# Performance work log

Hardware: AMD Instinct MI355X
Metric: run time of the kernel (lower is better)

## Reference

```python
import jax, jax.numpy as jnp
import numpy as np

BATCH, IN, HID, NCLS = 4096, 2048, 8192, 1000

def setup_inputs() -> dict:
    key = jax.random.key(0)
    kx, kk, kg = jax.random.split(key, 3)
    x = jax.random.normal(kx, (BATCH, IN), dtype=jnp.float32)
    # torch nn.Linear weights: kohonen [HID, IN], grossberg [NCLS, HID], init U(-1, 1)
    Wk = jax.random.uniform(kk, (HID, IN), dtype=jnp.float32, minval=-1.0, maxval=1.0)
    Wg = jax.random.uniform(kg, (NCLS, HID), dtype=jnp.float32, minval=-1.0, maxval=1.0)
    return {"x": x, "Wk": Wk, "Wg": Wg}

def reference(x, Wk, Wg):
    # L2-normalize each row
    xn = x / jnp.linalg.norm(x, axis=1, keepdims=True)  # [B, IN]
    kohonen_out = jnp.einsum('bi,hi->bh', xn, Wk)        # [B, HID]
    idx = jnp.argmax(kohonen_out, axis=1)                # [B] winner units
    # one-hot @ Wg.T == gather columns of Wg for winning units
    out = jnp.take(Wg, idx, axis=1).T                    # [B, NCLS]
    return out
```

## Files before the change

kernel.cpp:

```cpp
#include <hip/hip_runtime.h>
#include <stdint.h>

typedef unsigned int u32;
typedef unsigned long long u64;
typedef unsigned short u16;
typedef unsigned char u8;
typedef int intx8 __attribute__((ext_vector_type(8)));
typedef float floatx4 __attribute__((ext_vector_type(4)));

#define BATCH 4096
#define IN    2048
#define HID   8192
#define NCLS  1000

#define OFF_ROWKEY 0u
#define OFF_TOPK   32768u
#define OFF_X8     8421376u
#define OFF_WK8    16809984u
#define OFF_WGT    33587200u
#define TOTAL_FULL 66355200ull

__device__ __forceinline__ u32 fkey(float f) {
    u32 u = __float_as_uint(f);
    return (u & 0x80000000u) ? ~u : (u | 0x80000000u);
}
__device__ __forceinline__ float unfkey(u32 k) {
    return __uint_as_float((k & 0x80000000u) ? (k ^ 0x80000000u) : ~k);
}
__device__ __forceinline__ void ce32(u32& a, u32& b) {
    u32 mx = a > b ? a : b;
    u32 mn = a > b ? b : a;
    a = mx; b = mn;
}
__device__ __forceinline__ void ce(u64& a, u64& b) {
    u64 mx = a > b ? a : b;
    u64 mn = a > b ? b : a;
    a = mx; b = mn;
}

__global__ __launch_bounds__(256) void prep_kernel(
    const float* __restrict__ x, const float* __restrict__ Wk,
    const float* __restrict__ Wg,
    u8* __restrict__ x8, u8* __restrict__ wk8, float* __restrict__ WgT)
{
    __shared__ float t[32][33];
    const int bid = blockIdx.x;
    if (bid < 1024) {
        const int gid = bid * 256 + threadIdx.x;
        const int NSX = BATCH * IN / 16;
        const int NS  = NSX + HID * IN / 16;
        for (int s = gid; s < NS; s += 1024 * 256) {
            const float4* src; u8* dst;
            if (s < NSX) { src = (const float4*)x + (size_t)s * 4;  dst = x8  + (size_t)s * 16; }
            else { int u = s - NSX; src = (const float4*)Wk + (size_t)u * 4; dst = wk8 + (size_t)u * 16; }
            uint4 o;
            float4 f;
            int p;
            f = src[0];
            p = __builtin_amdgcn_cvt_pk_fp8_f32(f.x, f.y, 0, false);
            p = __builtin_amdgcn_cvt_pk_fp8_f32(f.z, f.w, p, true);  o.x = (u32)p;
            f = src[1];
            p = __builtin_amdgcn_cvt_pk_fp8_f32(f.x, f.y, 0, false);
            p = __builtin_amdgcn_cvt_pk_fp8_f32(f.z, f.w, p, true);  o.y = (u32)p;
            f = src[2];
            p = __builtin_amdgcn_cvt_pk_fp8_f32(f.x, f.y, 0, false);
            p = __builtin_amdgcn_cvt_pk_fp8_f32(f.z, f.w, p, true);  o.z = (u32)p;
            f = src[3];
            p = __builtin_amdgcn_cvt_pk_fp8_f32(f.x, f.y, 0, false);
            p = __builtin_amdgcn_cvt_pk_fp8_f32(f.z, f.w, p, true);  o.w = (u32)p;
            *(uint4*)dst = o;
        }
    } else {
        const int tb = bid - 1024;
        const int bx = (tb & 255) * 32;
        const int by = (tb >> 8) * 32;
        const int tx = threadIdx.x & 31, ty = threadIdx.x >> 5;
        #pragma unroll
        for (int i = 0; i < 32; i += 8) {
            int c = by + ty + i;
            t[ty + i][tx] = (c < NCLS) ? Wg[(size_t)c * HID + bx + tx] : 0.f;
        }
        __syncthreads();
        #pragma unroll
        for (int i = 0; i < 32; i += 8) {
            int c = by + tx;
            if (c < NCLS) WgT[(size_t)(bx + ty + i) * NCLS + by + tx] = t[tx][ty + i];
        }
    }
}

__global__ __launch_bounds__(256) void mfma_fp8_gemm_kernel(
    const u8* __restrict__ x8, const u8* __restrict__ wk8,
    u32* __restrict__ topk)
{
    __shared__ __align__(16) u8 At[128 * 128];
    __shared__ __align__(16) u8 Bt[128 * 128];

    const int tid  = threadIdx.x;
    const int lane = tid & 63;
    const int w    = tid >> 6;
    const int bm   = blockIdx.y * 128;
    const int bn   = blockIdx.x * 128;
    const int wrow = (w >> 1) * 64, wcol = (w & 1) * 64;
    const int m = lane & 15, q = lane >> 4;

    floatx4 acc[4][4];
    #pragma unroll
    for (int i = 0; i < 4; i++)
        #pragma unroll
        for (int j = 0; j < 4; j++)
            acc[i][j] = (floatx4){0.f, 0.f, 0.f, 0.f};

    const int srow = tid >> 3;
    const int soff = (((((tid >> 1) & 3) ^ (srow & 3)) * 2) + (tid & 1)) * 16;
    const u8* gxa = x8  + (size_t)(bm + srow) * IN + soff;
    const u8* gwb = wk8 + (size_t)(bn + srow) * IN + soff;

    const int foq = (q ^ (m & 3)) * 32;

    #pragma unroll 1
    for (int k0 = 0; k0 < IN; k0 += 128) {
        #pragma unroll
        for (int s = 0; s < 4; s++) {
            __builtin_amdgcn_global_load_lds(
                (const __attribute__((address_space(1))) u32*)(gxa + k0 + (size_t)s * 32 * IN),
                (__attribute__((address_space(3))) u32*)&At[s * 4096 + tid * 16], 16, 0, 0);
            __builtin_amdgcn_global_load_lds(
                (const __attribute__((address_space(1))) u32*)(gwb + k0 + (size_t)s * 32 * IN),
                (__attribute__((address_space(3))) u32*)&Bt[s * 4096 + tid * 16], 16, 0, 0);
        }
        __syncthreads();

        intx8 af[4];
        #pragma unroll
        for (int i = 0; i < 4; i++)
            af[i] = *(const intx8*)&At[(wrow + i * 16 + m) * 128 + foq];
        #pragma unroll
        for (int j = 0; j < 4; j++) {
            intx8 bf = *(const intx8*)&Bt[(wcol + j * 16 + m) * 128 + foq];
            #pragma unroll
            for (int i = 0; i < 4; i++)
                acc[i][j] = __builtin_amdgcn_mfma_scale_f32_16x16x128_f8f6f4(
                    af[i], bf, acc[i][j],
                    0, 0,
                    0, 0x7F,
                    0, 0x7F);
        }

        __syncthreads();
    }

    const int group = blockIdx.x * 2 + (wcol >> 6);
    #pragma unroll
    for (int i = 0; i < 4; i++) {
        #pragma unroll
        for (int r = 0; r < 4; r++) {
            u32 k0 = (fkey(acc[i][0][r]) & 0xFFFFFFC0u) | (0u << 4) | (u32)m;
            u32 k1 = (fkey(acc[i][1][r]) & 0xFFFFFFC0u) | (1u << 4) | (u32)m;
            u32 k2 = (fkey(acc[i][2][r]) & 0xFFFFFFC0u) | (2u << 4) | (u32)m;
            u32 k3 = (fkey(acc[i][3][r]) & 0xFFFFFFC0u) | (3u << 4) | (u32)m;
            ce32(k0, k1); ce32(k2, k3); ce32(k0, k2); ce32(k1, k3); ce32(k1, k2);
            #pragma unroll
            for (int off = 1; off < 16; off <<= 1) {
                u32 b0 = __shfl_xor(k0, off, 64);
                u32 b1 = __shfl_xor(k1, off, 64);
                u32 b2 = __shfl_xor(k2, off, 64);
                u32 b3 = __shfl_xor(k3, off, 64);
                u32 t0 = k0 > b3 ? k0 : b3;
                u32 t1 = k1 > b2 ? k1 : b2;
                u32 t2 = k2 > b1 ? k2 : b1;
                u32 t3 = k3 > b0 ? k3 : b0;
                ce32(t0, t2); ce32(t1, t3); ce32(t0, t1); ce32(t2, t3);
                k0 = t0; k1 = t1; k2 = t2; k3 = t3;
            }
            if (m == 0) {
                const int grow = bm + wrow + i * 16 + q * 4 + r;
                uint4 v; v.x = k0; v.y = k1; v.z = k2; v.w = k3;
                *(uint4*)&topk[(size_t)grow * 512 + group * 4] = v;
            }
        }
    }
}

__global__ __launch_bounds__(256) void scan_kernel(
    const u32* __restrict__ topk,
    const float* __restrict__ x, const float* __restrict__ Wk,
    const float* __restrict__ WgT, float* __restrict__ out)
{
    __shared__ u16 cand[4][48];
    const int wv   = threadIdx.x >> 6;
    const int lane = threadIdx.x & 63;
    const int row  = blockIdx.x * 4 + wv;

    const uint4* tp = (const uint4*)(topk + (size_t)row * 512);
    uint4 v0 = tp[lane];
    uint4 v1 = tp[lane + 64];

    u32 mx = v0.x > v1.x ? v0.x : v1.x;
    #pragma unroll
    for (int off = 1; off < 64; off <<= 1) {
        u32 o = __shfl_xor(mx, off, 64);
        if (o > mx) mx = o;
    }
    const float thr = unfkey(mx & 0xFFFFFFC0u) - 12.0f;

    int base = 0;
    const u32 ks[8] = {v0.x, v0.y, v0.z, v0.w, v1.x, v1.y, v1.z, v1.w};
    #pragma unroll
    for (int s = 0; s < 8; s++) {
        const int group = (s < 4) ? lane : (lane + 64);
        const u32 key = ks[s];
        const bool in = unfkey(key & 0xFFFFFFC0u) >= thr;
        const u64 msk = __ballot(in);
        if (in) {
            int rnk = base + __popcll(msk & ((1ull << lane) - 1ull));
            if (rnk < 48)
                cand[wv][rnk] = (u16)(group * 64 + (int)((key >> 4) & 3u) * 16 + (int)(key & 15u));
        }
        base += __popcll(msk);
    }
    const int n = min(base, 48);
    __builtin_amdgcn_wave_barrier();

    int col;
    if (n <= 1) {
        col = cand[wv][0];
    } else {
        const float4* xr = (const float4*)(x + (size_t)row * IN);
        float4 a[8];
        #pragma unroll
        for (int p = 0; p < 8; p++) a[p] = xr[p * 64 + lane];
        u64 best = 0ull;
        for (int c = 0; c < n; c++) {
            const int h = cand[wv][c];
            const float4* wr = (const float4*)(Wk + (size_t)h * IN);
            float s = 0.f;
            #pragma unroll
            for (int p = 0; p < 8; p++) {
                float4 b = wr[p * 64 + lane];
                s += a[p].x * b.x + a[p].y * b.y + a[p].z * b.z + a[p].w * b.w;
            }
            #pragma unroll
            for (int off = 1; off < 64; off <<= 1) s += __shfl_xor(s, off, 64);
            u64 key = ((u64)fkey(s) << 32) | (u64)(0x1FFFu - (u32)h);
            if (key > best) best = key;
        }
        col = 0x1FFF - (int)(best & 0xFFFFu);
    }

    const float4* src = (const float4*)(WgT + (size_t)col * NCLS);
    float4* dst = (float4*)(out + (size_t)row * NCLS);
    for (int t = lane; t < NCLS / 4; t += 64) dst[t] = src[t];
}

__global__ void init_ws_kernel(u64* rowkey) {
    int i = blockIdx.x * blockDim.x + threadIdx.x;
    if (i < BATCH) rowkey[i] = 0ULL;
}

__global__ __launch_bounds__(256) void gemm_argmax_kernel(
    const float* __restrict__ x, const float* __restrict__ Wk,
    u64* __restrict__ rowkey)
{
    __shared__ __align__(16) float As[32 * 64];
    __shared__ __align__(16) float Bs[32 * 64];
    const int tid = threadIdx.x;
    const int bm = blockIdx.y * 64, bn = blockIdx.x * 64;
    const int tx = tid & 15, ty = tid >> 4;
    float acc[4][4];
    #pragma unroll
    for (int i = 0; i < 4; i++)
        #pragma unroll
        for (int j = 0; j < 4; j++) acc[i][j] = 0.f;
    const int r0 = tid >> 3, q0 = tid & 7;
    const int r1 = (tid + 256) >> 3, q1 = (tid + 256) & 7;
    const float* xA0 = &x[(size_t)(bm + r0) * IN + q0 * 4];
    const float* xA1 = &x[(size_t)(bm + r1) * IN + q1 * 4];
    const float* wB0 = &Wk[(size_t)(bn + r0) * IN + q0 * 4];
    const float* wB1 = &Wk[(size_t)(bn + r1) * IN + q1 * 4];
    for (int k0 = 0; k0 < IN; k0 += 32) {
        float4 a0 = *(const float4*)(xA0 + k0);
        float4 a1 = *(const float4*)(xA1 + k0);
        float4 b0 = *(const float4*)(wB0 + k0);
        float4 b1 = *(const float4*)(wB1 + k0);
        __syncthreads();
        As[(q0 * 4 + 0) * 64 + r0] = a0.x; As[(q0 * 4 + 1) * 64 + r0] = a0.y;
        As[(q0 * 4 + 2) * 64 + r0] = a0.z; As[(q0 * 4 + 3) * 64 + r0] = a0.w;
        As[(q1 * 4 + 0) * 64 + r1] = a1.x; As[(q1 * 4 + 1) * 64 + r1] = a1.y;
        As[(q1 * 4 + 2) * 64 + r1] = a1.z; As[(q1 * 4 + 3) * 64 + r1] = a1.w;
        Bs[(q0 * 4 + 0) * 64 + r0] = b0.x; Bs[(q0 * 4 + 1) * 64 + r0] = b0.y;
        Bs[(q0 * 4 + 2) * 64 + r0] = b0.z; Bs[(q0 * 4 + 3) * 64 + r0] = b0.w;
        Bs[(q1 * 4 + 0) * 64 + r1] = b1.x; Bs[(q1 * 4 + 1) * 64 + r1] = b1.y;
        Bs[(q1 * 4 + 2) * 64 + r1] = b1.z; Bs[(q1 * 4 + 3) * 64 + r1] = b1.w;
        __syncthreads();
        #pragma unroll
        for (int k = 0; k < 32; k++) {
            float4 av = *(const float4*)&As[k * 64 + ty * 4];
            float4 bv = *(const float4*)&Bs[k * 64 + tx * 4];
            acc[0][0] += av.x * bv.x; acc[0][1] += av.x * bv.y;
            acc[0][2] += av.x * bv.z; acc[0][3] += av.x * bv.w;
            acc[1][0] += av.y * bv.x; acc[1][1] += av.y * bv.y;
            acc[1][2] += av.y * bv.z; acc[1][3] += av.y * bv.w;
            acc[2][0] += av.z * bv.x; acc[2][1] += av.z * bv.y;
            acc[2][2] += av.z * bv.z; acc[2][3] += av.z * bv.w;
            acc[3][0] += av.w * bv.x; acc[3][1] += av.w * bv.y;
            acc[3][2] += av.w * bv.z; acc[3][3] += av.w * bv.w;
        }
    }
    #pragma unroll
    for (int i = 0; i < 4; i++) {
        const int row = bm + ty * 4 + i;
        u64 best = 0ULL;
        #pragma unroll
        for (int j = 0; j < 4; j++) {
            const int col = bn + tx * 4 + j;
            u64 p = ((u64)fkey(acc[i][j]) << 32) | (u64)(0x1FFFu - (unsigned)col);
            if (p > best) best = p;
        }
        #pragma unroll
        for (int off = 1; off < 16; off <<= 1) {
            u64 other = __shfl_xor(best, off, 64);
            if (other > best) best = other;
        }
        if (tx == 0) atomicMax(&rowkey[row], best);
    }
}

__global__ __launch_bounds__(256) void gather_kernel(
    const u64* __restrict__ rowkey, const float* __restrict__ Wg,
    float* __restrict__ out)
{
    const int b = blockIdx.y;
    const int c = blockIdx.x * 256 + threadIdx.x;
    if (c >= NCLS) return;
    const int col = 0x1FFF - (int)(rowkey[b] & 0xFFFFFFFFu);
    out[(size_t)b * NCLS + c] = Wg[(size_t)c * HID + col];
}

extern "C" void kernel_launch(void* const* d_in, const int* in_sizes, int n_in,
                              void* d_out, int out_size, void* d_ws, size_t ws_size,
                              hipStream_t stream) {
    const float* x  = (const float*)d_in[0];
    const float* Wk = (const float*)d_in[1];
    const float* Wg = (const float*)d_in[2];
    float* out = (float*)d_out;
    char* ws = (char*)d_ws;

    if (ws_size >= TOTAL_FULL) {
        u32* topk  = (u32*)(ws + OFF_TOPK);
        u8*  x8    = (u8*)(ws + OFF_X8);
        u8*  wk8   = (u8*)(ws + OFF_WK8);
        float* WgT = (float*)(ws + OFF_WGT);

        hipLaunchKernelGGL(prep_kernel, dim3(1024 + 8192), dim3(256), 0, stream,
                           x, Wk, Wg, x8, wk8, WgT);
        hipLaunchKernelGGL(mfma_fp8_gemm_kernel, dim3(HID / 128, BATCH / 128), dim3(256), 0, stream,
                           x8, wk8, topk);
        hipLaunchKernelGGL(scan_kernel, dim3(BATCH / 4), dim3(256), 0, stream,
                           topk, x, Wk, WgT, out);
    } else {
        u64* rowkey = (u64*)(ws + OFF_ROWKEY);
        hipLaunchKernelGGL(init_ws_kernel, dim3(16), dim3(256), 0, stream, rowkey);
        hipLaunchKernelGGL(gemm_argmax_kernel, dim3(HID / 64, BATCH / 64), dim3(256), 0, stream,
                           x, Wk, rowkey);
        hipLaunchKernelGGL(gather_kernel, dim3(4, BATCH), dim3(256), 0, stream,
                           rowkey, Wg, out);
    }
}
```

Before: 304.6 us.

## Triple-buffer LDS and widen FP8 GEMM tile to 128x256 with 512 threads

Restructures the FP8 MFMA GEMM into a 3-stage LDS ring buffer (144KB) with global-to-LDS prefetch two K-steps ahead. Loads are split across two half-iterations interleaved with MFMA groups, using s_setprio and fine-grained vmcnt waits in place of full __syncthreads. The block tile grows to 128x256 with 8 waves, and the topk group indexing changes to match. This aims to hide global load latency and cut synchronization stalls, at the cost of large LDS use (one block per CU) and more fragile manual waitcnt logic.

Measured after the change: 323.8 us. 1.06x slower.

```diff
diff --git a/kernel.cpp b/kernel.cpp
--- a/kernel.cpp
+++ b/kernel.cpp
@@ -30,11 +30,6 @@
 __device__ __forceinline__ void ce32(u32& a, u32& b) {
     u32 mx = a > b ? a : b;
     u32 mn = a > b ? b : a;
-    a = mx; b = mn;
-}
-__device__ __forceinline__ void ce(u64& a, u64& b) {
-    u64 mx = a > b ? a : b;
-    u64 mn = a > b ? b : a;
     a = mx; b = mn;
 }
 
@@ -89,19 +84,23 @@
     }
 }
 
-__global__ __launch_bounds__(256) void mfma_fp8_gemm_kernel(
+#define STAGE(gsrc, ldsoff) \
+    __builtin_amdgcn_global_load_lds((const __attribute__((address_space(1))) u32*)(gsrc), \
+        (__attribute__((address_space(3))) u32*)&LDS[ldsoff], 16, 0, 0)
+
+__global__ __launch_bounds__(512) void mfma_fp8_gemm_kernel(
     const u8* __restrict__ x8, const u8* __restrict__ wk8,
     u32* __restrict__ topk)
 {
-    __shared__ __align__(16) u8 At[128 * 128];
-    __shared__ __align__(16) u8 Bt[128 * 128];
+    __shared__ __align__(16) u8 LDS[3 * 49152];
 
     const int tid  = threadIdx.x;
     const int lane = tid & 63;
     const int w    = tid >> 6;
     const int bm   = blockIdx.y * 128;
-    const int bn   = blockIdx.x * 128;
-    const int wrow = (w >> 1) * 64, wcol = (w & 1) * 64;
+    const int bn   = blockIdx.x * 256;
+    const int wrow = (w >> 2) * 64;
+    const int wcol = (w & 3) * 64;
     const int m = lane & 15, q = lane >> 4;
 
     floatx4 acc[4][4];
@@ -115,42 +114,90 @@
     const int soff = (((((tid >> 1) & 3) ^ (srow & 3)) * 2) + (tid & 1)) * 16;
     const u8* gxa = x8  + (size_t)(bm + srow) * IN + soff;
     const u8* gwb = wk8 + (size_t)(bn + srow) * IN + soff;
-
-    const int foq = (q ^ (m & 3)) * 32;
+    const u32 ldst = (u32)tid * 16;
+
+    const int foq  = (q ^ (m & 3)) * 32;
+    const u32 aoff = (u32)(wrow + m) * 128 + (u32)foq;
+    const u32 boff = 16384u + (u32)(wcol + m) * 128 + (u32)foq;
+
+    STAGE(gxa,                            0u         + ldst);
+    STAGE(gxa +  64 * (size_t)IN,         8192u      + ldst);
+    STAGE(gwb,                            16384u     + ldst);
+    STAGE(gwb +  64 * (size_t)IN,         24576u     + ldst);
+    STAGE(gwb + 128 * (size_t)IN,         32768u     + ldst);
+    STAGE(gwb + 192 * (size_t)IN,         40960u     + ldst);
+    __builtin_amdgcn_sched_barrier(0);
+    STAGE(gxa + 128,                      49152u          + ldst);
+    STAGE(gxa +  64 * (size_t)IN + 128,   49152u + 8192u  + ldst);
+    STAGE(gwb + 128,                      49152u + 16384u + ldst);
+    STAGE(gwb +  64 * (size_t)IN + 128,   49152u + 24576u + ldst);
+    STAGE(gwb + 128 * (size_t)IN + 128,   49152u + 32768u + ldst);
+    STAGE(gwb + 192 * (size_t)IN + 128,   49152u + 40960u + ldst);
+    asm volatile("s_waitcnt vmcnt(6)" ::: "memory");
+    __builtin_amdgcn_s_barrier();
+
+    u32 rb = 0u;
+    u32 sb = 98304u;
 
     #pragma unroll 1
-    for (int k0 = 0; k0 < IN; k0 += 128) {
-        #pragma unroll
-        for (int s = 0; s < 4; s++) {
-            __builtin_amdgcn_global_load_lds(
-                (const __attribute__((address_space(1))) u32*)(gxa + k0 + (size_t)s * 32 * IN),
-                (__attribute__((address_space(3))) u32*)&At[s * 4096 + tid * 16], 16, 0, 0);
-            __builtin_amdgcn_global_load_lds(
-                (const __attribute__((address_space(1))) u32*)(gwb + k0 + (size_t)s * 32 * IN),
-                (__attribute__((address_space(3))) u32*)&Bt[s * 4096 + tid * 16], 16, 0, 0);
-        }
-        __syncthreads();
-
+    for (int kt = 0; kt < 16; ++kt) {
+        const size_t ko2 = (size_t)(kt + 2) * 128;
         intx8 af[4];
         #pragma unroll
         for (int i = 0; i < 4; i++)
-            af[i] = *(const intx8*)&At[(wrow + i * 16 + m) * 128 + foq];
-        #pragma unroll
-        for (int j = 0; j < 4; j++) {
-            intx8 bf = *(const intx8*)&Bt[(wcol + j * 16 + m) * 128 + foq];
-            #pragma unroll
-            for (int i = 0; i < 4; i++)
-                acc[i][j] = __builtin_amdgcn_mfma_scale_f32_16x16x128_f8f6f4(
-                    af[i], bf, acc[i][j],
-                    0, 0,
-                    0, 0x7F,
-                    0, 0x7F);
-        }
-
-        __syncthreads();
-    }
-
-    const int group = blockIdx.x * 2 + (wcol >> 6);
+            af[i] = *(const intx8*)&LDS[rb + aoff + (u32)i * 2048u];
+        intx8 bf0 = *(const intx8*)&LDS[rb + boff];
+        intx8 bf1 = *(const intx8*)&LDS[rb + boff + 2048u];
+        if (kt < 14) {
+            STAGE(gxa + ko2,                      sb          + ldst);
+            STAGE(gxa +  64 * (size_t)IN + ko2,   sb + 8192u  + ldst);
+            STAGE(gwb + ko2,                      sb + 16384u + ldst);
+        }
+        asm volatile("" ::: "memory");
+        __builtin_amdgcn_s_barrier();
+        asm volatile("s_waitcnt lgkmcnt(0)" ::: "memory");
+        __builtin_amdgcn_sched_barrier(0);
+        __builtin_amdgcn_s_setprio(1);
+        #pragma unroll
+        for (int i = 0; i < 4; i++)
+            acc[i][0] = __builtin_amdgcn_mfma_scale_f32_16x16x128_f8f6f4(
+                af[i], bf0, acc[i][0], 0, 0, 0, 0x7F, 0, 0x7F);
+        #pragma unroll
+        for (int i = 0; i < 4; i++)
+            acc[i][1] = __builtin_amdgcn_mfma_scale_f32_16x16x128_f8f6f4(
+                af[i], bf1, acc[i][1], 0, 0, 0, 0x7F, 0, 0x7F);
+        __builtin_amdgcn_s_setprio(0);
+        asm volatile("" ::: "memory");
+        __builtin_amdgcn_s_barrier();
+        intx8 bf2 = *(const intx8*)&LDS[rb + boff + 4096u];
+        intx8 bf3 = *(const intx8*)&LDS[rb + boff + 6144u];
+        if (kt < 14) {
+            STAGE(gwb +  64 * (size_t)IN + ko2,   sb + 24576u + ldst);
+            STAGE(gwb + 128 * (size_t)IN + ko2,   sb + 32768u + ldst);
+            STAGE(gwb + 192 * (size_t)IN + ko2,   sb + 40960u + ldst);
+        }
+        asm volatile("" ::: "memory");
+        __builtin_amdgcn_s_barrier();
+        asm volatile("s_waitcnt lgkmcnt(0)" ::: "memory");
+        __builtin_amdgcn_sched_barrier(0);
+        __builtin_amdgcn_s_setprio(1);
+        #pragma unroll
+        for (int i = 0; i < 4; i++)
+            acc[i][2] = __builtin_amdgcn_mfma_scale_f32_16x16x128_f8f6f4(
+                af[i], bf2, acc[i][2], 0, 0, 0, 0x7F, 0, 0x7F);
+        #pragma unroll
+        for (int i = 0; i < 4; i++)
+            acc[i][3] = __builtin_amdgcn_mfma_scale_f32_16x16x128_f8f6f4(
+                af[i], bf3, acc[i][3], 0, 0, 0, 0x7F, 0, 0x7F);
+        __builtin_amdgcn_s_setprio(0);
+        if (kt < 13)       asm volatile("s_waitcnt vmcnt(6)" ::: "memory");
+        else               asm volatile("s_waitcnt vmcnt(0)" ::: "memory");
+        __builtin_amdgcn_s_barrier();
+        rb = (rb == 98304u) ? 0u : rb + 49152u;
+        sb = (sb == 98304u) ? 0u : sb + 49152u;
+    }
+
+    const int group = blockIdx.x * 4 + (w & 3);
     #pragma unroll
     for (int i = 0; i < 4; i++) {
         #pragma unroll
@@ -354,7 +401,7 @@
 
         hipLaunchKernelGGL(prep_kernel, dim3(1024 + 8192), dim3(256), 0, stream,
                            x, Wk, Wg, x8, wk8, WgT);
-        hipLaunchKernelGGL(mfma_fp8_gemm_kernel, dim3(HID / 128, BATCH / 128), dim3(256), 0, stream,
+        hipLaunchKernelGGL(mfma_fp8_gemm_kernel, dim3(HID / 256, BATCH / 128), dim3(512), 0, stream,
                            x8, wk8, topk);
         hipLaunchKernelGGL(scan_kernel, dim3(BATCH / 4), dim3(256), 0, stream,
                            topk, x, Wk, WgT, out);
```
